# Performance work log

Hardware: AMD Instinct MI355X
Metric: run time of the kernel (lower is better)

## Reference

```python
import jax, jax.numpy as jnp
import numpy as np

D_IN = 1024
D_OUT = 1024
SEQ = 4096


def setup_inputs() -> dict:
    key = jax.random.key(0)
    kx, kq, kk, kv = jax.random.split(key, 4)
    s = 1.0 / np.sqrt(D_IN)
    return {
        "x": jax.random.normal(kx, (SEQ, D_IN), dtype=jnp.float32),
        # torch Linear weights: shape [d_out, d_in], y = x @ W.T
        "Wq": jax.random.uniform(kq, (D_OUT, D_IN), jnp.float32, -s, s),
        "Wk": jax.random.uniform(kk, (D_OUT, D_IN), jnp.float32, -s, s),
        "Wv": jax.random.uniform(kv, (D_OUT, D_IN), jnp.float32, -s, s),
    }


def reference(x, Wq, Wk, Wv):
    # QKV projections (no bias)
    q = x @ Wq.T  # [N, d_out]
    k = x @ Wk.T
    v = x @ Wv.T
    scale = 1.0 / jnp.sqrt(jnp.asarray(k.shape[-1], x.dtype))
    att = jax.nn.softmax((q @ k.T) * scale, axis=-1)  # [N, N]
    return att @ v  # [N, d_out]
```

## Files before the change

kernel.cpp:

```cpp
#include <hip/hip_runtime.h>
#include <hip/hip_bf16.h>
#include <math.h>

typedef __attribute__((ext_vector_type(8))) short short8;
typedef __attribute__((ext_vector_type(4))) float floatx4;

static __device__ __forceinline__ unsigned short f2bf(float f) {
    union { float f; unsigned int u; } a; a.f = f;
    unsigned int u = a.u;
    return (unsigned short)((u + 0x7FFFu + ((u >> 16) & 1u)) >> 16);
}

static __device__ __forceinline__ void cvt8(const float* __restrict__ src,
                                            unsigned short* __restrict__ dst, int i) {
    float4 v0 = *(const float4*)(src + i);
    float4 v1 = *(const float4*)(src + i + 4);
    ushort4 o0, o1;
    o0.x = f2bf(v0.x); o0.y = f2bf(v0.y); o0.z = f2bf(v0.z); o0.w = f2bf(v0.w);
    o1.x = f2bf(v1.x); o1.y = f2bf(v1.y); o1.z = f2bf(v1.z); o1.w = f2bf(v1.w);
    *(ushort4*)(dst + i) = o0;
    *(ushort4*)(dst + i + 4) = o1;
}

__global__ __launch_bounds__(256)
void cvt_x_zero(const float* __restrict__ src, unsigned short* __restrict__ dst,
                int n, float* __restrict__ l) {
    if ((int)blockIdx.x == gridDim.x - 1) {
        float4 z = {0.f, 0.f, 0.f, 0.f};
        #pragma unroll
        for (int c = 0; c < 4; c++)
            *(float4*)(l + threadIdx.x * 16 + c * 4) = z;
        return;
    }
    int i = (blockIdx.x * 256 + threadIdx.x) * 8;
    if (i < n) cvt8(src, dst, i);
}

struct W3 { const float* s[3]; unsigned short* d[3]; };
__global__ __launch_bounds__(256)
void cvt_w3(W3 a, int n) {
    int i = (blockIdx.x * 256 + threadIdx.x) * 8;
    if (i < n) cvt8(a.s[blockIdx.z], a.d[blockIdx.z], i);
}

template<int BM, int BN, int BK, int TI, int TJ, int WCOLS>
__device__ __forceinline__ void gemm_core(const unsigned short* __restrict__ A,
                                          const unsigned short* __restrict__ B,
                                          int lda, int k_begin, int k_end,
                                          unsigned short* sA, unsigned short* sB,
                                          floatx4 (&acc)[TI][TJ],
                                          int bm, int bn)
{
    constexpr int CPR = BK / 8;
    constexpr int RPR = 2048 / BK;
    const int t    = threadIdx.x;
    const int wave = t >> 6;
    const int lane = t & 63;
    const int wm = (wave / WCOLS) * (TI * 16);
    const int wn = (wave % WCOLS) * (TJ * 16);

    const int srow   = t / CPR;
    const int schunk = t % CPR;
    const int gchunk = schunk ^ (srow & (CPR - 1));
    const int lm  = lane & 15;
    const int swz = lm & (CPR - 1);

    for (int k0 = k_begin; k0 < k_end; k0 += BK) {
        __syncthreads();
        #pragma unroll
        for (int r = 0; r < (BM * BK) / 2048; r++) {
            const unsigned short* gA =
                A + (size_t)(bm + srow + r * RPR) * lda + k0 + gchunk * 8;
            __builtin_amdgcn_global_load_lds(
                (const __attribute__((address_space(1))) void*)gA,
                (__attribute__((address_space(3))) void*)((char*)sA + wave * 1024 + r * 4096),
                16, 0, 0);
        }
        #pragma unroll
        for (int r = 0; r < (BN * BK) / 2048; r++) {
            const unsigned short* gB =
                B + (size_t)(bn + srow + r * RPR) * lda + k0 + gchunk * 8;
            __builtin_amdgcn_global_load_lds(
                (const __attribute__((address_space(1))) void*)gB,
                (__attribute__((address_space(3))) void*)((char*)sB + wave * 1024 + r * 4096),
                16, 0, 0);
        }
        __syncthreads();

        #pragma unroll
        for (int kk = 0; kk < BK; kk += 32) {
            const int c  = (kk >> 3) + (lane >> 4);
            const int ce = ((c ^ swz) << 3);
            short8 a_frag[TI], b_frag[TJ];
            #pragma unroll
            for (int i = 0; i < TI; i++)
                a_frag[i] = *(const short8*)&sA[(wm + i * 16 + lm) * BK + ce];
            #pragma unroll
            for (int j = 0; j < TJ; j++)
                b_frag[j] = *(const short8*)&sB[(wn + j * 16 + lm) * BK + ce];
            #pragma unroll
            for (int i = 0; i < TI; i++)
                #pragma unroll
                for (int j = 0; j < TJ; j++)
                    acc[i][j] = __builtin_amdgcn_mfma_f32_16x16x32_bf16(
                        a_frag[i], b_frag[j], acc[i][j], 0, 0, 0);
        }
    }
}


struct P3 { const unsigned short* W[3]; unsigned short* O[3]; };
__global__ __launch_bounds__(256)
void proj3(const unsigned short* __restrict__ xb, P3 a) {
    __shared__ unsigned short sA[64 * 64];
    __shared__ unsigned short sB[128 * 64];
    const int z = blockIdx.z;
    const unsigned short* B = a.W[z];
    unsigned short* O = a.O[z];
    const bool trans = (z == 2);
    const int ldc = trans ? 4096 : 1024;
    const float scale = (z == 0) ? 0.03125f : 1.0f;

    floatx4 acc[4][2];
    #pragma unroll
    for (int i = 0; i < 4; i++)
        #pragma unroll
        for (int j = 0; j < 2; j++) { floatx4 zz = {0.f,0.f,0.f,0.f}; acc[i][j] = zz; }

    const int bm = blockIdx.y * 64, bn = blockIdx.x * 128;
    gemm_core<64, 128, 64, 4, 2, 4>(xb, B, 1024, 0, 1024, sA, sB, acc, bm, bn);

    const int lane = threadIdx.x & 63, wave = threadIdx.x >> 6;
    const int wn = (wave & 3) * 32;
    const int lm = lane & 15, rq = (lane >> 4) * 4;
    #pragma unroll
    for (int i = 0; i < 4; i++)
        #pragma unroll
        for (int j = 0; j < 2; j++) {
            int tm = bm + i * 16 + rq;
            int tn = bn + wn + j * 16 + lm;
            #pragma unroll
            for (int r = 0; r < 4; r++) {
                unsigned short h = f2bf(acc[i][j][r] * scale);
                size_t idx = trans ? ((size_t)tn * ldc + (tm + r))
                                   : ((size_t)(tm + r) * ldc + tn);
                O[idx] = h;
            }
        }
}

__global__ __launch_bounds__(256)
void gemm_ps(const unsigned short* __restrict__ q, const unsigned short* __restrict__ k,
             unsigned short* __restrict__ Pm, float* __restrict__ l) {
    __shared__ unsigned short sA[128 * 128];
    __shared__ unsigned short sB[128 * 128];

    floatx4 acc[4][4];
    #pragma unroll
    for (int i = 0; i < 4; i++)
        #pragma unroll
        for (int j = 0; j < 4; j++) { floatx4 zz = {0.f,0.f,0.f,0.f}; acc[i][j] = zz; }

    const int bm = blockIdx.y * 128, bn = blockIdx.x * 128;
    gemm_core<128, 128, 128, 4, 4, 2>(q, k, 1024, 0, 1024, sA, sB, acc, bm, bn);

    const int lane = threadIdx.x & 63, wave = threadIdx.x >> 6;
    const int wm = (wave >> 1) * 64, wn = (wave & 1) * 64;
    const int lm = lane & 15, rq = (lane >> 4) * 4;
    #pragma unroll
    for (int i = 0; i < 4; i++) {
        #pragma unroll
        for (int r = 0; r < 4; r++) {
            int row = bm + wm + i * 16 + rq + r;
            float rs = 0.f;
            #pragma unroll
            for (int j = 0; j < 4; j++) {
                float e = __expf(acc[i][j][r]);
                rs += e;
                int tn = bn + wn + j * 16 + lm;
                Pm[(size_t)row * 4096 + tn] = f2bf(e);
            }
            rs += __shfl_xor(rs, 1);
            rs += __shfl_xor(rs, 2);
            rs += __shfl_xor(rs, 4);
            rs += __shfl_xor(rs, 8);
            if (lm == 0) atomicAdd(l + row, rs);
        }
    }
}

__global__ __launch_bounds__(256)
void gemm_osplit(const unsigned short* __restrict__ Pm, const unsigned short* __restrict__ vT,
                 float* __restrict__ Opart) {
    __shared__ unsigned short sA[64 * 128];
    __shared__ unsigned short sB[128 * 128];

    floatx4 acc[4][2];
    #pragma unroll
    for (int i = 0; i < 4; i++)
        #pragma unroll
        for (int j = 0; j < 2; j++) { floatx4 zz = {0.f,0.f,0.f,0.f}; acc[i][j] = zz; }

    const int z = blockIdx.z;
    const int bm = blockIdx.y * 64, bn = blockIdx.x * 128;
    gemm_core<64, 128, 128, 4, 2, 4>(Pm, vT, 4096, z * 2048, (z + 1) * 2048,
                                     sA, sB, acc, bm, bn);

    float* Op = Opart + (size_t)z * (4096 * 1024);
    const int lane = threadIdx.x & 63, wave = threadIdx.x >> 6;
    const int wn = (wave & 3) * 32;
    const int lm = lane & 15, rq = (lane >> 4) * 4;
    #pragma unroll
    for (int i = 0; i < 4; i++)
        #pragma unroll
        for (int j = 0; j < 2; j++) {
            int tm = bm + i * 16 + rq;
            int tn = bn + wn + j * 16 + lm;
            #pragma unroll
            for (int r = 0; r < 4; r++)
                Op[(size_t)(tm + r) * 1024 + tn] = acc[i][j][r];
        }
}

__global__ __launch_bounds__(256)
void reduce_scale(const float* __restrict__ Op, const float* __restrict__ l,
                  float* __restrict__ out) {
    int i = (blockIdx.x * 256 + threadIdx.x) * 4;
    float4 a = *(const float4*)(Op + i);
    float4 b = *(const float4*)(Op + 4096 * 1024 + i);
    float inv = 1.0f / l[i >> 10];
    float4 o;
    o.x = (a.x + b.x) * inv; o.y = (a.y + b.y) * inv;
    o.z = (a.z + b.z) * inv; o.w = (a.w + b.w) * inv;
    *(float4*)(out + i) = o;
}

extern "C" void kernel_launch(void* const* d_in, const int* in_sizes, int n_in,
                              void* d_out, int out_size, void* d_ws, size_t ws_size,
                              hipStream_t stream) {
    const float* x  = (const float*)d_in[0];
    const float* Wq = (const float*)d_in[1];
    const float* Wk = (const float*)d_in[2];
    const float* Wv = (const float*)d_in[3];
    float* out = (float*)d_out;

    const int SEQ = 4096, D = 1024;
    char* ws = (char*)d_ws;
    const size_t MB = 1u << 20;
    unsigned short* vTb = (unsigned short*)(ws);
    unsigned short* xb  = (unsigned short*)(ws + 8 * MB);
    unsigned short* Wqb = (unsigned short*)(ws + 16 * MB);
    unsigned short* Wkb = (unsigned short*)(ws + 18 * MB);
    unsigned short* Wvb = (unsigned short*)(ws + 20 * MB);
    unsigned short* qb  = (unsigned short*)(ws + 22 * MB);
    unsigned short* kb  = (unsigned short*)(ws + 30 * MB);
    unsigned short* P   = (unsigned short*)(ws + 38 * MB);
    float*          l   = (float*)(ws + 70 * MB);
    float*          Opart = (float*)(ws + 72 * MB);

    dim3 blk(256);
    cvt_x_zero<<<(SEQ * D) / 2048 + 1, blk, 0, stream>>>(x, xb, SEQ * D, l);
    W3 w3 = {{Wq, Wk, Wv}, {Wqb, Wkb, Wvb}};
    cvt_w3<<<dim3((D * D) / 2048, 1, 3), blk, 0, stream>>>(w3, D * D);

    P3 p3 = {{Wqb, Wkb, Wvb}, {qb, kb, vTb}};
    proj3<<<dim3(D / 128, SEQ / 64, 3), blk, 0, stream>>>(xb, p3);

    gemm_ps<<<dim3(SEQ / 128, SEQ / 128), blk, 0, stream>>>(qb, kb, P, l);

    gemm_osplit<<<dim3(D / 128, SEQ / 64, 2), blk, 0, stream>>>(P, vTb, Opart);

    reduce_scale<<<(SEQ * D) / 1024, blk, 0, stream>>>(Opart, l, out);
}
```

Before: 236.3 us.

## Remap GEMM tiles per XCD and fuse split-K reduction into the P·V epilogue

The score GEMM now uses a 1D grid whose block index is remapped so that each XCD works on a compact 16x8 patch of output tiles, improving L2 reuse of q and k rows. The P·V GEMM drops the two-way K split and the separate reduce kernel. Each block now runs the full K=4096 loop and applies the 1/l normalization directly in its epilogue, which removes the partial-output write and reread. The cost is half as many blocks for the P·V stage (512) and longer per-block K loops, which may lower occupancy and latency hiding.

Measured after the change: 227.4 us. 3.7% less time.

```diff
diff --git a/kernel.cpp b/kernel.cpp
--- a/kernel.cpp
+++ b/kernel.cpp
@@ -155,13 +155,19 @@
     __shared__ unsigned short sA[128 * 128];
     __shared__ unsigned short sB[128 * 128];
 
+    const int lid = blockIdx.x;
+    const int xcd = lid & 7;
+    const int i8  = lid >> 3;
+    const int by  = (xcd & 1) * 16 + (i8 & 15);
+    const int bx  = (xcd >> 1) * 8 + (i8 >> 4);
+
     floatx4 acc[4][4];
     #pragma unroll
     for (int i = 0; i < 4; i++)
         #pragma unroll
         for (int j = 0; j < 4; j++) { floatx4 zz = {0.f,0.f,0.f,0.f}; acc[i][j] = zz; }
 
-    const int bm = blockIdx.y * 128, bn = blockIdx.x * 128;
+    const int bm = by * 128, bn = bx * 128;
     gemm_core<128, 128, 128, 4, 4, 2>(q, k, 1024, 0, 1024, sA, sB, acc, bm, bn);
 
     const int lane = threadIdx.x & 63, wave = threadIdx.x >> 6;
@@ -190,49 +196,43 @@
 }
 
 __global__ __launch_bounds__(256)
-void gemm_osplit(const unsigned short* __restrict__ Pm, const unsigned short* __restrict__ vT,
-                 float* __restrict__ Opart) {
+void gemm_o(const unsigned short* __restrict__ Pm, const unsigned short* __restrict__ vT,
+            const float* __restrict__ l, float* __restrict__ out) {
     __shared__ unsigned short sA[64 * 128];
     __shared__ unsigned short sB[128 * 128];
 
+    const int lid = blockIdx.x;
+    const int r8  = lid & 7;
+    const int w64 = lid & 63;
+    const int c   = w64 >> 3;
+    const int row = (lid >> 6) * 8 + r8;
+
     floatx4 acc[4][2];
     #pragma unroll
     for (int i = 0; i < 4; i++)
         #pragma unroll
         for (int j = 0; j < 2; j++) { floatx4 zz = {0.f,0.f,0.f,0.f}; acc[i][j] = zz; }
 
-    const int z = blockIdx.z;
-    const int bm = blockIdx.y * 64, bn = blockIdx.x * 128;
-    gemm_core<64, 128, 128, 4, 2, 4>(Pm, vT, 4096, z * 2048, (z + 1) * 2048,
-                                     sA, sB, acc, bm, bn);
-
-    float* Op = Opart + (size_t)z * (4096 * 1024);
+    const int bm = row * 64, bn = c * 128;
+    gemm_core<64, 128, 128, 4, 2, 4>(Pm, vT, 4096, 0, 4096, sA, sB, acc, bm, bn);
+
     const int lane = threadIdx.x & 63, wave = threadIdx.x >> 6;
     const int wn = (wave & 3) * 32;
     const int lm = lane & 15, rq = (lane >> 4) * 4;
     #pragma unroll
-    for (int i = 0; i < 4; i++)
+    for (int i = 0; i < 4; i++) {
+        int tm = bm + i * 16 + rq;
+        float inv[4];
+        #pragma unroll
+        for (int r = 0; r < 4; r++) inv[r] = 1.0f / l[tm + r];
         #pragma unroll
         for (int j = 0; j < 2; j++) {
-            int tm = bm + i * 16 + rq;
             int tn = bn + wn + j * 16 + lm;
             #pragma unroll
             for (int r = 0; r < 4; r++)
-                Op[(size_t)(tm + r) * 1024 + tn] = acc[i][j][r];
-        }
-}
-
-__global__ __launch_bounds__(256)
-void reduce_scale(const float* __restrict__ Op, const float* __restrict__ l,
-                  float* __restrict__ out) {
-    int i = (blockIdx.x * 256 + threadIdx.x) * 4;
-    float4 a = *(const float4*)(Op + i);
-    float4 b = *(const float4*)(Op + 4096 * 1024 + i);
-    float inv = 1.0f / l[i >> 10];
-    float4 o;
-    o.x = (a.x + b.x) * inv; o.y = (a.y + b.y) * inv;
-    o.z = (a.z + b.z) * inv; o.w = (a.w + b.w) * inv;
-    *(float4*)(out + i) = o;
+                out[(size_t)(tm + r) * 1024 + tn] = acc[i][j][r] * inv[r];
+        }
+    }
 }
 
 extern "C" void kernel_launch(void* const* d_in, const int* in_sizes, int n_in,
@@ -256,7 +256,6 @@
     unsigned short* kb  = (unsigned short*)(ws + 30 * MB);
     unsigned short* P   = (unsigned short*)(ws + 38 * MB);
     float*          l   = (float*)(ws + 70 * MB);
-    float*          Opart = (float*)(ws + 72 * MB);
 
     dim3 blk(256);
     cvt_x_zero<<<(SEQ * D) / 2048 + 1, blk, 0, stream>>>(x, xb, SEQ * D, l);
@@ -266,9 +265,7 @@
     P3 p3 = {{Wqb, Wkb, Wvb}, {qb, kb, vTb}};
     proj3<<<dim3(D / 128, SEQ / 64, 3), blk, 0, stream>>>(xb, p3);
 
-    gemm_ps<<<dim3(SEQ / 128, SEQ / 128), blk, 0, stream>>>(qb, kb, P, l);
-
-    gemm_osplit<<<dim3(D / 128, SEQ / 64, 2), blk, 0, stream>>>(P, vTb, Opart);
-
-    reduce_scale<<<(SEQ * D) / 1024, blk, 0, stream>>>(Opart, l, out);
-}
+    gemm_ps<<<dim3(1024), blk, 0, stream>>>(qb, kb, P, l);
+
+    gemm_o<<<dim3(512), blk, 0, stream>>>(P, vTb, l, out);
+}
```
